# Kernel optimization log

Hardware: AMD Instinct MI355X
Metric: run time of the kernel (lower is better)

## Reference

```python
import jax, jax.numpy as jnp
import numpy as np

D_MODEL = 1024
NUM_HEADS = 16
HEAD_DIM = D_MODEL // NUM_HEADS
SCALE = HEAD_DIM ** -0.5
BATCH = 4096
N_MODULES = 8


def setup_inputs() -> dict:
    key = jax.random.key(0)
    ks = jax.random.split(key, 7)
    s = 1.0 / np.sqrt(D_MODEL)
    return {
        "query": jax.random.normal(ks[0], (BATCH, D_MODEL), jnp.float32),
        "kv_stack": jax.random.normal(ks[1], (N_MODULES, BATCH, D_MODEL), jnp.float32),
        "Wq": jax.random.normal(ks[2], (D_MODEL, D_MODEL), jnp.float32) * s,
        "Wk": jax.random.normal(ks[3], (D_MODEL, D_MODEL), jnp.float32) * s,
        "Wv": jax.random.normal(ks[4], (D_MODEL, D_MODEL), jnp.float32) * s,
        "Wo": jax.random.normal(ks[5], (D_MODEL, D_MODEL), jnp.float32) * s,
        "bo": jnp.zeros((D_MODEL,), jnp.float32),
    }


def reference(query, kv_stack, Wq, Wk, Wv, Wo, bo):
    # query: [B, D]; kv_stack: [M, B, D] (stacked module representations)
    B = query.shape[0]
    M = kv_stack.shape[0]
    # projections (nn.Linear: x @ W.T), split into heads; seq_len == 1
    q = (query @ Wq.T).reshape(B, NUM_HEADS, HEAD_DIM)            # [B,H,hd]
    k = jnp.einsum("mbd,ed->mbe", kv_stack, Wk).reshape(M, B, NUM_HEADS, HEAD_DIM)
    v = jnp.einsum("mbd,ed->mbe", kv_stack, Wv).reshape(M, B, NUM_HEADS, HEAD_DIM)
    # scores over the single kv position: [M,B,H,1]
    scores = jnp.einsum("bhd,mbhd->mbh", q, k)[..., None] * SCALE
    attn_weights = jax.nn.softmax(scores, axis=-1)  # softmax over size-1 axis -> ones
    attn_output = attn_weights * v                   # [M,B,H,hd] (dropout is eval/no-op)
    attn_output = attn_output.reshape(M, B, D_MODEL)
    out = jnp.einsum("mbe,oe->mbo", attn_output, Wo) + bo + query  # residual per module
    return out  # [M, B, D] (stacked in kv order instead of the dict)
```

## Files before the change

### kernel.cpp

```cpp
#include <hip/hip_runtime.h>
#include <hip/hip_bf16.h>


typedef __attribute__((ext_vector_type(4))) float f32x4;
typedef __attribute__((ext_vector_type(8))) short short8;

#define D_MODEL 1024
#define BATCH   4096
#define M_ROWS  32768

__device__ __forceinline__ short f2bf(float f) {
    union { float f; unsigned u; } x; x.f = f;
    unsigned r = (x.u + 0x7fffu + ((x.u >> 16) & 1u)) >> 16;
    return (short)r;
}

__device__ __forceinline__ unsigned bfpk(float lo, float hi) {
    __hip_bfloat162 h = __float22bfloat162_rn(make_float2(lo, hi));
    unsigned u; __builtin_memcpy(&u, &h, 4); return u;
}

__device__ __forceinline__ short8 cvt8(float4 a, float4 b) {
    union { unsigned u[4]; short8 s; } r;
    r.u[0] = bfpk(a.x, a.y);
    r.u[1] = bfpk(a.z, a.w);
    r.u[2] = bfpk(b.x, b.y);
    r.u[3] = bfpk(b.z, b.w);
    return r.s;
}

__global__ __launch_bounds__(256) void fuse_w_kernel(
        const float* __restrict__ Wo, const float* __restrict__ Wv,
        short* __restrict__ Cw) {
    __shared__ __align__(16) short Ash[64][32];
    __shared__ __align__(16) short Bsh[64][32];
    const int t = threadIdx.x;
    const int lane = t & 63;
    const int w = t >> 6;
    const int wr = w >> 1, wc = w & 1;
    const int brow = blockIdx.y * 64;
    const int bcol = blockIdx.x * 64;

    f32x4 acc[2][2];
#pragma unroll
    for (int m = 0; m < 2; ++m)
#pragma unroll
        for (int n = 0; n < 2; ++n) acc[m][n] = (f32x4)(0.0f);

    for (int kt = 0; kt < 32; ++kt) {
        const float* ga = Wo + (size_t)(brow + (t >> 2)) * D_MODEL + kt * 32 + (t & 3) * 8;
        float4 a0 = *(const float4*)ga;
        float4 a1 = *(const float4*)(ga + 4);
        float4 bv[2];
#pragma unroll
        for (int j = 0; j < 2; ++j) {
            int lin = j * 256 + t;
            int e = lin >> 4, c4 = lin & 15;
            bv[j] = *(const float4*)(Wv + (size_t)(kt * 32 + e) * D_MODEL + bcol + c4 * 4);
        }
        *reinterpret_cast<short8*>(&Ash[t >> 2][(t & 3) * 8]) = cvt8(a0, a1);
#pragma unroll
        for (int j = 0; j < 2; ++j) {
            int lin = j * 256 + t;
            int e = lin >> 4, c4 = lin & 15;
            int d = c4 * 4;
            Bsh[d + 0][e] = f2bf(bv[j].x);
            Bsh[d + 1][e] = f2bf(bv[j].y);
            Bsh[d + 2][e] = f2bf(bv[j].z);
            Bsh[d + 3][e] = f2bf(bv[j].w);
        }
        __syncthreads();
        {
            const int r = lane & 15, q = lane >> 4;
            short8 af[2], bfr[2];
#pragma unroll
            for (int m = 0; m < 2; ++m)
                af[m] = *reinterpret_cast<const short8*>(&Ash[wr * 32 + m * 16 + r][q * 8]);
#pragma unroll
            for (int n = 0; n < 2; ++n)
                bfr[n] = *reinterpret_cast<const short8*>(&Bsh[wc * 32 + n * 16 + r][q * 8]);
#pragma unroll
            for (int m = 0; m < 2; ++m)
#pragma unroll
                for (int n = 0; n < 2; ++n)
                    acc[m][n] = __builtin_amdgcn_mfma_f32_16x16x32_bf16(
                        af[m], bfr[n], acc[m][n], 0, 0, 0);
        }
        __syncthreads();
    }

    const int r = lane & 15, q = lane >> 4;
#pragma unroll
    for (int m = 0; m < 2; ++m)
#pragma unroll
        for (int n = 0; n < 2; ++n)
#pragma unroll
            for (int j = 0; j < 4; ++j) {
                int o = brow + wr * 32 + m * 16 + q * 4 + j;
                int d = bcol + wc * 32 + n * 16 + r;
                Cw[(size_t)o * D_MODEL + d] = f2bf(acc[m][n][j]);
            }
}

__global__ __launch_bounds__(256, 4) void attn_gemm_kernel(
        const float* __restrict__ kv, const float* __restrict__ query,
        const short* __restrict__ Cw, const float* __restrict__ bo,
        float* __restrict__ out) {
    __shared__ __align__(16) float Afs[64][64];
    __shared__ __align__(16) short Bsh[128][64];
    const int t = threadIdx.x;
    const int lane = t & 63;
    const int w = t >> 6;
    const int wr = w >> 1, wc = w & 1;
    const int r = lane & 15, q = lane >> 4;

    const int L = blockIdx.x;
    const int x = L & 7, j5 = L >> 3;
    const int bx = j5 & 7;
    const int rt = (j5 >> 3) * 8 + x;
    const int brow = rt * 64;

    f32x4 acc[2][4];
#pragma unroll
    for (int m = 0; m < 2; ++m)
#pragma unroll
        for (int n = 0; n < 4; ++n) acc[m][n] = (f32x4)(0.0f);

    for (int kt = 0; kt < 16; ++kt) {
#pragma unroll
        for (int i = 0; i < 4; ++i) {
            int chunk = i * 256 + t;
            int rl = chunk >> 4, d = chunk & 15;
            int cs = d ^ (rl & 7);
            const float* g = kv + (size_t)(brow + rl) * D_MODEL + kt * 64 + cs * 4;
            __builtin_amdgcn_global_load_lds(
                (const __attribute__((address_space(1))) void*)g,
                (__attribute__((address_space(3))) void*)
                    ((char*)&Afs[0][0] + i * 4096 + w * 1024),
                16, 0, 0);
        }
#pragma unroll
        for (int i = 0; i < 4; ++i) {
            int chunk = i * 256 + t;
            int rl = chunk >> 3, d = chunk & 7;
            int cs = d ^ (rl & 7);
            const short* g = Cw + (size_t)(bx * 128 + rl) * D_MODEL + kt * 64 + cs * 8;
            __builtin_amdgcn_global_load_lds(
                (const __attribute__((address_space(1))) void*)g,
                (__attribute__((address_space(3))) void*)
                    ((char*)&Bsh[0][0] + i * 4096 + w * 1024),
                16, 0, 0);
        }
        __syncthreads();
#pragma unroll
        for (int s = 0; s < 2; ++s) {
            short8 af[2], bfr[4];
#pragma unroll
            for (int m = 0; m < 2; ++m) {
                int row = wr * 32 + m * 16 + r;
                int c0 = (s * 8 + q * 2) ^ (row & 7);
                int c1 = (s * 8 + q * 2 + 1) ^ (row & 7);
                float4 lo = *(const float4*)&Afs[row][c0 * 4];
                float4 hi = *(const float4*)&Afs[row][c1 * 4];
                af[m] = cvt8(lo, hi);
            }
#pragma unroll
            for (int n = 0; n < 4; ++n) {
                int row = wc * 64 + n * 16 + r;
                int c = (s * 4 + q) ^ (row & 7);
                bfr[n] = *reinterpret_cast<const short8*>(&Bsh[row][c * 8]);
            }
#pragma unroll
            for (int m = 0; m < 2; ++m)
#pragma unroll
                for (int n = 0; n < 4; ++n)
                    acc[m][n] = __builtin_amdgcn_mfma_f32_16x16x32_bf16(
                        af[m], bfr[n], acc[m][n], 0, 0, 0);
        }
        __syncthreads();
    }

#pragma unroll
    for (int n = 0; n < 4; ++n) {
        int o = bx * 128 + wc * 64 + n * 16 + r;
        float bov = bo[o];
#pragma unroll
        for (int m = 0; m < 2; ++m) {
            int gb = brow + wr * 32 + m * 16 + q * 4;
#pragma unroll
            for (int j = 0; j < 4; ++j) {
                int grow = gb + j;
                out[(size_t)grow * D_MODEL + o] =
                    acc[m][n][j] + bov +
                    query[(size_t)(grow & (BATCH - 1)) * D_MODEL + o];
            }
        }
    }
}

extern "C" void kernel_launch(void* const* d_in, const int* in_sizes, int n_in,
                              void* d_out, int out_size, void* d_ws, size_t ws_size,
                              hipStream_t stream) {
    int kv_i = 1, q_i = 0, bo_i = 6;
    int w_i[4] = {2, 3, 4, 5};
    int nw = 0;
    for (int i = 0; i < n_in; ++i) {
        long s = in_sizes[i];
        if (s == 33554432) kv_i = i;
        else if (s == 4194304) q_i = i;
        else if (s == 1024) bo_i = i;
        else if (s == 1048576 && nw < 4) w_i[nw++] = i;
    }
    const float* query = (const float*)d_in[q_i];
    const float* kv    = (const float*)d_in[kv_i];
    const float* Wv    = (const float*)d_in[w_i[2]];
    const float* Wo    = (const float*)d_in[w_i[3]];
    const float* bo    = (const float*)d_in[bo_i];
    short* Cw  = (short*)d_ws;
    float* out = (float*)d_out;

    fuse_w_kernel<<<dim3(16, 16), dim3(256), 0, stream>>>(Wo, Wv, Cw);
    attn_gemm_kernel<<<dim3(4096), dim3(256), 0, stream>>>(kv, query, Cw, bo, out);
}
```

Baseline: 175.7 us.

## Prefetch A tile to registers and convert to bf16 once before LDS

The kv (A) operand is now loaded with ordinary vector loads into registers one k-tile ahead, converted to bf16 once per element, and stored into a swizzled bf16 LDS tile. Previously the fp32 tile went straight to LDS via global_load_lds and was converted to bf16 inside the MFMA loop by each consuming wave. The change halves A's LDS footprint and removes the redundant per-wave conversion, and the register prefetch overlaps the next tile's global load with the current MFMAs. The cost is more registers for the prefetch buffers, which may hurt occupancy under launch_bounds(256,4).

```diff
diff --git a/kernel.cpp b/kernel.cpp
--- a/kernel.cpp
+++ b/kernel.cpp
@@ -106,7 +106,7 @@
         const float* __restrict__ kv, const float* __restrict__ query,
         const short* __restrict__ Cw, const float* __restrict__ bo,
         float* __restrict__ out) {
-    __shared__ __align__(16) float Afs[64][64];
+    __shared__ __align__(16) short Abs[64][64];
     __shared__ __align__(16) short Bsh[128][64];
     const int t = threadIdx.x;
     const int lane = t & 63;
@@ -126,19 +126,24 @@
 #pragma unroll
         for (int n = 0; n < 4; ++n) acc[m][n] = (f32x4)(0.0f);
 
-    for (int kt = 0; kt < 16; ++kt) {
-#pragma unroll
-        for (int i = 0; i < 4; ++i) {
-            int chunk = i * 256 + t;
-            int rl = chunk >> 4, d = chunk & 15;
-            int cs = d ^ (rl & 7);
-            const float* g = kv + (size_t)(brow + rl) * D_MODEL + kt * 64 + cs * 4;
-            __builtin_amdgcn_global_load_lds(
-                (const __attribute__((address_space(1))) void*)g,
-                (__attribute__((address_space(3))) void*)
-                    ((char*)&Afs[0][0] + i * 4096 + w * 1024),
-                16, 0, 0);
-        }
+    const int arow = t >> 2;
+    const float* abase = kv + (size_t)(brow + arow) * D_MODEL + 16 * (t & 3);
+    float4 ar[4];
+
+    auto load_a = [&](int kt) {
+        const float* g = abase + kt * 64;
+        ar[0] = *(const float4*)(g + 0);
+        ar[1] = *(const float4*)(g + 4);
+        ar[2] = *(const float4*)(g + 8);
+        ar[3] = *(const float4*)(g + 12);
+    };
+    auto write_a = [&]() {
+        int c0 = (2 * (t & 3)) ^ (arow & 7);
+        int c1 = (2 * (t & 3) + 1) ^ (arow & 7);
+        *reinterpret_cast<short8*>(&Abs[arow][c0 * 8]) = cvt8(ar[0], ar[1]);
+        *reinterpret_cast<short8*>(&Abs[arow][c1 * 8]) = cvt8(ar[2], ar[3]);
+    };
+    auto glds_b = [&](int kt) {
 #pragma unroll
         for (int i = 0; i < 4; ++i) {
             int chunk = i * 256 + t;
@@ -151,18 +156,16 @@
                     ((char*)&Bsh[0][0] + i * 4096 + w * 1024),
                 16, 0, 0);
         }
-        __syncthreads();
+    };
+    auto compute = [&]() {
 #pragma unroll
         for (int s = 0; s < 2; ++s) {
             short8 af[2], bfr[4];
 #pragma unroll
             for (int m = 0; m < 2; ++m) {
                 int row = wr * 32 + m * 16 + r;
-                int c0 = (s * 8 + q * 2) ^ (row & 7);
-                int c1 = (s * 8 + q * 2 + 1) ^ (row & 7);
-                float4 lo = *(const float4*)&Afs[row][c0 * 4];
-                float4 hi = *(const float4*)&Afs[row][c1 * 4];
-                af[m] = cvt8(lo, hi);
+                int c = (s * 4 + q) ^ (row & 7);
+                af[m] = *reinterpret_cast<const short8*>(&Abs[row][c * 8]);
             }
 #pragma unroll
             for (int n = 0; n < 4; ++n) {
@@ -177,6 +180,15 @@
                     acc[m][n] = __builtin_amdgcn_mfma_f32_16x16x32_bf16(
                         af[m], bfr[n], acc[m][n], 0, 0, 0);
         }
+    };
+
+    load_a(0);
+    for (int kt = 0; kt < 16; ++kt) {
+        glds_b(kt);
+        write_a();
+        __syncthreads();
+        if (kt < 15) load_a(kt + 1);
+        compute();
         __syncthreads();
     }
 
```

New measurement: 183.3 us. +4.3%, slower.

## Double-buffer LDS tiles to overlap global loads with MFMA compute

Applied to the files above, without the earlier changes.

Splits the main GEMM loop into stage and compute steps over two LDS buffers. The loads for the next k-tile are issued before computing the current one, with an explicit vmcnt wait and raw barriers replacing __syncthreads. The aim is to hide global-to-LDS latency behind the matrix math. In exchange, LDS per block doubles to 64KB, which likely cuts resident blocks per CU below the requested four.

```diff
diff --git a/kernel.cpp b/kernel.cpp
--- a/kernel.cpp
+++ b/kernel.cpp
@@ -106,8 +106,8 @@
         const float* __restrict__ kv, const float* __restrict__ query,
         const short* __restrict__ Cw, const float* __restrict__ bo,
         float* __restrict__ out) {
-    __shared__ __align__(16) float Afs[64][64];
-    __shared__ __align__(16) short Bsh[128][64];
+    __shared__ __align__(16) float Afs[2][64][64];
+    __shared__ __align__(16) short Bsh[2][128][64];
     const int t = threadIdx.x;
     const int lane = t & 63;
     const int w = t >> 6;
@@ -126,7 +126,7 @@
 #pragma unroll
         for (int n = 0; n < 4; ++n) acc[m][n] = (f32x4)(0.0f);
 
-    for (int kt = 0; kt < 16; ++kt) {
+    auto stage = [&](int kt, int buf) {
 #pragma unroll
         for (int i = 0; i < 4; ++i) {
             int chunk = i * 256 + t;
@@ -136,7 +136,7 @@
             __builtin_amdgcn_global_load_lds(
                 (const __attribute__((address_space(1))) void*)g,
                 (__attribute__((address_space(3))) void*)
-                    ((char*)&Afs[0][0] + i * 4096 + w * 1024),
+                    ((char*)&Afs[buf][0][0] + i * 4096 + w * 1024),
                 16, 0, 0);
         }
 #pragma unroll
@@ -148,10 +148,11 @@
             __builtin_amdgcn_global_load_lds(
                 (const __attribute__((address_space(1))) void*)g,
                 (__attribute__((address_space(3))) void*)
-                    ((char*)&Bsh[0][0] + i * 4096 + w * 1024),
+                    ((char*)&Bsh[buf][0][0] + i * 4096 + w * 1024),
                 16, 0, 0);
         }
-        __syncthreads();
+    };
+    auto compute = [&](int buf) {
 #pragma unroll
         for (int s = 0; s < 2; ++s) {
             short8 af[2], bfr[4];
@@ -160,15 +161,15 @@
                 int row = wr * 32 + m * 16 + r;
                 int c0 = (s * 8 + q * 2) ^ (row & 7);
                 int c1 = (s * 8 + q * 2 + 1) ^ (row & 7);
-                float4 lo = *(const float4*)&Afs[row][c0 * 4];
-                float4 hi = *(const float4*)&Afs[row][c1 * 4];
+                float4 lo = *(const float4*)&Afs[buf][row][c0 * 4];
+                float4 hi = *(const float4*)&Afs[buf][row][c1 * 4];
                 af[m] = cvt8(lo, hi);
             }
 #pragma unroll
             for (int n = 0; n < 4; ++n) {
                 int row = wc * 64 + n * 16 + r;
                 int c = (s * 4 + q) ^ (row & 7);
-                bfr[n] = *reinterpret_cast<const short8*>(&Bsh[row][c * 8]);
+                bfr[n] = *reinterpret_cast<const short8*>(&Bsh[buf][row][c * 8]);
             }
 #pragma unroll
             for (int m = 0; m < 2; ++m)
@@ -177,7 +178,20 @@
                     acc[m][n] = __builtin_amdgcn_mfma_f32_16x16x32_bf16(
                         af[m], bfr[n], acc[m][n], 0, 0, 0);
         }
-        __syncthreads();
+    };
+
+    stage(0, 0);
+    for (int kt = 0; kt < 16; ++kt) {
+        const int cur = kt & 1;
+        if (kt < 15) {
+            stage(kt + 1, cur ^ 1);
+            asm volatile("s_waitcnt vmcnt(8)" ::: "memory");
+        } else {
+            asm volatile("s_waitcnt vmcnt(0)" ::: "memory");
+        }
+        __builtin_amdgcn_s_barrier();
+        compute(cur);
+        __builtin_amdgcn_s_barrier();
     }
 
 #pragma unroll
```

Result: slower. 236.0 us (+34.3%).

## Pre-convert kv to bf16 and triple-buffer the attention GEMM

Applied to the files above, without the earlier changes.

Adds a separate pass that converts the whole fp32 kv stack to bf16 in workspace. The main GEMM then streams bf16 A and B tiles through a three-stage asynchronous LDS pipeline paced by explicit vmcnt waits, instead of loading fp32 tiles, converting them in registers and running a single buffer per step. This is meant to halve the A-operand load traffic inside the GEMM and overlap loads with MFMA work, at the cost of an extra full read and write pass over kv. The original fp32 path remains as a fallback when the workspace is too small.

```diff
diff --git a/kernel.cpp b/kernel.cpp
--- a/kernel.cpp
+++ b/kernel.cpp
@@ -27,6 +27,18 @@
     r.u[2] = bfpk(b.x, b.y);
     r.u[3] = bfpk(b.z, b.w);
     return r.s;
+}
+
+__global__ __launch_bounds__(256) void cvt_kv_kernel(
+        const float* __restrict__ in, short* __restrict__ outb) {
+    const long n8 = (long)M_ROWS * D_MODEL / 8;
+    long i = (long)blockIdx.x * 256 + threadIdx.x;
+    const long stride = (long)gridDim.x * 256;
+    for (; i < n8; i += stride) {
+        const float4* p = (const float4*)(in + i * 8);
+        float4 a = p[0], b = p[1];
+        *reinterpret_cast<short8*>(outb + i * 8) = cvt8(a, b);
+    }
 }
 
 __global__ __launch_bounds__(256) void fuse_w_kernel(
@@ -102,7 +114,112 @@
             }
 }
 
-__global__ __launch_bounds__(256, 4) void attn_gemm_kernel(
+__global__ __launch_bounds__(256, 4) void attn_gemm_bf16(
+        const short* __restrict__ kvb, const float* __restrict__ query,
+        const short* __restrict__ Cw, const float* __restrict__ bo,
+        float* __restrict__ out) {
+    __shared__ __align__(16) short Afs[3][64][32];
+    __shared__ __align__(16) short Bsh[3][128][32];
+    const int t = threadIdx.x;
+    const int lane = t & 63;
+    const int w = t >> 6;
+    const int wr = w >> 1, wc = w & 1;
+    const int r = lane & 15, q = lane >> 4;
+
+    const int L = blockIdx.x;
+    const int x = L & 7, j5 = L >> 3;
+    const int bx = j5 & 7;
+    const int rt = (j5 >> 3) * 8 + x;
+    const int brow = rt * 64;
+
+    f32x4 acc[2][4];
+#pragma unroll
+    for (int m = 0; m < 2; ++m)
+#pragma unroll
+        for (int n = 0; n < 4; ++n) acc[m][n] = (f32x4)(0.0f);
+
+    auto stage = [&](int kt, int buf) {
+        {
+            int rl = t >> 2, d = t & 3;
+            int cs = d ^ (rl & 3);
+            const short* g = kvb + (size_t)(brow + rl) * D_MODEL + kt * 32 + cs * 8;
+            __builtin_amdgcn_global_load_lds(
+                (const __attribute__((address_space(1))) void*)g,
+                (__attribute__((address_space(3))) void*)
+                    ((char*)&Afs[buf][0][0] + w * 1024),
+                16, 0, 0);
+        }
+#pragma unroll
+        for (int i = 0; i < 2; ++i) {
+            int chunk = i * 256 + t;
+            int rl = chunk >> 2, d = chunk & 3;
+            int cs = d ^ (rl & 3);
+            const short* g = Cw + (size_t)(bx * 128 + rl) * D_MODEL + kt * 32 + cs * 8;
+            __builtin_amdgcn_global_load_lds(
+                (const __attribute__((address_space(1))) void*)g,
+                (__attribute__((address_space(3))) void*)
+                    ((char*)&Bsh[buf][0][0] + i * 4096 + w * 1024),
+                16, 0, 0);
+        }
+    };
+    auto compute = [&](int buf) {
+        short8 af[2], bfr[4];
+#pragma unroll
+        for (int m = 0; m < 2; ++m) {
+            int row = wr * 32 + m * 16 + r;
+            int c = q ^ (row & 3);
+            af[m] = *reinterpret_cast<const short8*>(&Afs[buf][row][c * 8]);
+        }
+#pragma unroll
+        for (int n = 0; n < 4; ++n) {
+            int row = wc * 64 + n * 16 + r;
+            int c = q ^ (row & 3);
+            bfr[n] = *reinterpret_cast<const short8*>(&Bsh[buf][row][c * 8]);
+        }
+#pragma unroll
+        for (int m = 0; m < 2; ++m)
+#pragma unroll
+            for (int n = 0; n < 4; ++n)
+                acc[m][n] = __builtin_amdgcn_mfma_f32_16x16x32_bf16(
+                    af[m], bfr[n], acc[m][n], 0, 0, 0);
+    };
+
+    stage(0, 0);
+    stage(1, 1);
+    for (int kt = 0; kt < 32; ++kt) {
+        const int bsel = kt % 3;
+        if (kt < 30) {
+            stage(kt + 2, (kt + 2) % 3);
+            asm volatile("s_waitcnt vmcnt(6)" ::: "memory");
+        } else if (kt == 30) {
+            asm volatile("s_waitcnt vmcnt(3)" ::: "memory");
+        } else {
+            asm volatile("s_waitcnt vmcnt(0)" ::: "memory");
+        }
+        __builtin_amdgcn_s_barrier();
+        compute(bsel);
+        __builtin_amdgcn_s_barrier();
+    }
+
+#pragma unroll
+    for (int n = 0; n < 4; ++n) {
+        int o = bx * 128 + wc * 64 + n * 16 + r;
+        float bov = bo[o];
+#pragma unroll
+        for (int m = 0; m < 2; ++m) {
+            int gb = brow + wr * 32 + m * 16 + q * 4;
+#pragma unroll
+            for (int j = 0; j < 4; ++j) {
+                int grow = gb + j;
+                out[(size_t)grow * D_MODEL + o] =
+                    acc[m][n][j] + bov +
+                    query[(size_t)(grow & (BATCH - 1)) * D_MODEL + o];
+            }
+        }
+    }
+}
+
+__global__ __launch_bounds__(256, 4) void attn_gemm_f32(
         const float* __restrict__ kv, const float* __restrict__ query,
         const short* __restrict__ Cw, const float* __restrict__ bo,
         float* __restrict__ out) {
@@ -220,5 +337,13 @@
     float* out = (float*)d_out;
 
     fuse_w_kernel<<<dim3(16, 16), dim3(256), 0, stream>>>(Wo, Wv, Cw);
-    attn_gemm_kernel<<<dim3(4096), dim3(256), 0, stream>>>(kv, query, Cw, bo, out);
-}
+
+    const size_t need = (size_t)2 * 1024 * 1024 + (size_t)M_ROWS * D_MODEL * 2;
+    if (ws_size >= need) {
+        short* kvb = (short*)((char*)d_ws + 2 * 1024 * 1024);
+        cvt_kv_kernel<<<dim3(2048), dim3(256), 0, stream>>>(kv, kvb);
+        attn_gemm_bf16<<<dim3(4096), dim3(256), 0, stream>>>(kvb, query, Cw, bo, out);
+    } else {
+        attn_gemm_f32<<<dim3(4096), dim3(256), 0, stream>>>(kv, query, Cw, bo, out);
+    }
+}
```

Result: slower. 194.6 us (+10.8%).
